# Optimization experiments

Measured on AMD Instinct MI355X. Metric: run time of the kernel, lower is better.

The kernel has to match this reference:

```python
import jax, jax.numpy as jnp
import numpy as np

N_NODES = 50000
D_IN = 256
D_OUT = 128
N_POS = 1600000   # positive edges used for GCN aggregation
N_PRED = 500000   # edges to score


def setup_inputs() -> dict:
    key = jax.random.key(0)
    ks = jax.random.split(key, 6)
    x = jax.random.normal(ks[0], (N_NODES, D_IN), dtype=jnp.float32)
    pos_edge_index = jax.random.randint(ks[1], (2, N_POS), 0, N_NODES)
    edge_index = jax.random.randint(ks[2], (2, N_PRED), 0, N_NODES)
    # init_linear: Linear(d_in, d_in); stored as (in, out) so fwd is x @ W1 + b1
    W1 = jax.random.normal(ks[3], (D_IN, D_IN), dtype=jnp.float32) / np.sqrt(D_IN).astype(np.float32)
    b1 = jnp.zeros((D_IN,), dtype=jnp.float32)
    # GCNConv weight (in, out) and bias
    Wc = jax.random.normal(ks[4], (D_IN, D_OUT), dtype=jnp.float32) / np.sqrt(D_IN).astype(np.float32)
    bc = jnp.zeros((D_OUT,), dtype=jnp.float32)
    return dict(x=x, edge_index=edge_index, pos_edge_index=pos_edge_index,
                W1=W1, b1=b1, Wc=Wc, bc=bc)


def reference(x, edge_index, pos_edge_index, W1, b1, Wc, bc):
    n = x.shape[0]
    # init_linear
    h = x @ W1 + b1                                  # [N, D_IN]
    # GCNConv: linear transform first, then normalized scatter-add aggregation
    h = h @ Wc                                       # [N, D_OUT]
    # add self-loops (PyG GCNConv default add_self_loops=True, edge_weight=1)
    loops = jnp.arange(n, dtype=pos_edge_index.dtype)
    row = jnp.concatenate([pos_edge_index[0], loops])  # source
    col = jnp.concatenate([pos_edge_index[1], loops])  # target (aggregation)
    # symmetric normalization: deg over target, norm = d^-1/2[row]*d^-1/2[col]
    deg = jax.ops.segment_sum(jnp.ones_like(col, dtype=h.dtype), col, num_segments=n)
    dinv = jnp.where(deg > 0, jax.lax.rsqrt(deg), 0.0)
    norm = dinv[row] * dinv[col]                     # [E+N]
    msgs = h[row] * norm[:, None]                    # gather + scale
    out = jax.ops.segment_sum(msgs, col, num_segments=n) + bc  # scatter-add + bias
    # edge dot-product scoring
    logits = (out[edge_index[0]] * out[edge_index[1]]).sum(axis=-1)  # [N_PRED]
    return logits
```

## Files before the change

kernel.cpp:

```cpp
#include <hip/hip_runtime.h>

#define N_NODES 50000
#define D_IN 256
#define D_OUT 128
#define N_POS 1600000
#define N_PRED 500000

#define G_BUCKETS 782
#define GPAD 1024
#define SB 640
#define CHUNK 2500
#define CAP 4096
#define GEMM_BLOCKS 782
#define QPRED 125000

#define NT 4
#define TSZ 12500
#define NPB 32
#define AGGB 1563

typedef __attribute__((ext_vector_type(8))) short short8;
typedef __attribute__((ext_vector_type(4))) float f32x4;

__device__ __forceinline__ unsigned short f2bf(float f) {
    unsigned int u = __float_as_uint(f);
    u += 0x7FFFu + ((u >> 16) & 1u);
    return (unsigned short)(u >> 16);
}
__device__ __forceinline__ unsigned int pk2(float a, float b) {
    unsigned int ua = __float_as_uint(a), ub = __float_as_uint(b);
    ua += 0x7FFFu + ((ua >> 16) & 1u);
    ub += 0x7FFFu + ((ub >> 16) & 1u);
    return (ua >> 16) | (ub & 0xFFFF0000u);
}
__device__ __forceinline__ float bflo(unsigned int u) { return __uint_as_float(u << 16); }
__device__ __forceinline__ float bfhi(unsigned int u) { return __uint_as_float(u & 0xFFFF0000u); }

__device__ __forceinline__ float dot8(uint4 ua, uint4 ub) {
    return bflo(ua.x) * bflo(ub.x) + bfhi(ua.x) * bfhi(ub.x)
         + bflo(ua.y) * bflo(ub.y) + bfhi(ua.y) * bfhi(ub.y)
         + bflo(ua.z) * bflo(ub.z) + bfhi(ua.z) * bfhi(ub.z)
         + bflo(ua.w) * bflo(ub.w) + bfhi(ua.w) * bfhi(ub.w);
}

__global__ void fuse_weights_k(const float* __restrict__ W1, const float* __restrict__ Wc,
                               const float* __restrict__ b1,
                               unsigned short* __restrict__ Bp, float* __restrict__ bf,
                               int* __restrict__ bfill) {
    if (blockIdx.x == 128) {
        for (int g = threadIdx.x; g < G_BUCKETS; g += 256) bfill[g] = g * CAP;
        return;
    }
    int gid = blockIdx.x * blockDim.x + threadIdx.x;
    int k = gid >> 7;
    int n = gid & 127;
    float acc = 0.f;
    #pragma unroll 4
    for (int kk = 0; kk < D_IN; ++kk)
        acc += W1[k * D_IN + kk] * Wc[kk * D_OUT + n];
    int ks = k >> 5, q = (k >> 3) & 3, jj = k & 7;
    int nt = n >> 4, nl = n & 15;
    int lane = q * 16 + nl;
    Bp[(((long)(ks * 8 + nt)) * 64 + lane) * 8 + jj] = f2bf(acc);
    if (gid < D_OUT) {
        float accb = 0.f;
        for (int kk = 0; kk < D_IN; ++kk)
            accb += b1[kk] * Wc[kk * D_OUT + gid];
        bf[gid] = accb;
    }
}

__global__ __launch_bounds__(256) void scatter_gemm_k(const int* __restrict__ row,
                                                      const int* __restrict__ col,
                                                      int* __restrict__ bfill,
                                                      unsigned int* __restrict__ eb,
                                                      const float* __restrict__ x,
                                                      const uint4* __restrict__ Bp,
                                                      const float* __restrict__ bf,
                                                      unsigned short* __restrict__ hsb) {
    __shared__ __align__(16) char smem[27456];
    if (blockIdx.x < GEMM_BLOCKS) {
        const int wave = threadIdx.x >> 6;
        const int lane = threadIdx.x & 63;
        const int q    = lane >> 4;
        const int ml   = lane & 15;
        const int m0   = blockIdx.x * 64 + wave * 16;

        f32x4 acc[8];
        #pragma unroll
        for (int t = 0; t < 8; ++t) acc[t] = (f32x4){0.f, 0.f, 0.f, 0.f};

        long arow = m0 + ml; if (arow > N_NODES - 1) arow = N_NODES - 1;
        const float* xrow = x + arow * D_IN + q * 8;

        #pragma unroll
        for (int ks = 0; ks < 8; ++ks) {
            float4 xa = *(const float4*)(xrow + ks * 32);
            float4 xb = *(const float4*)(xrow + ks * 32 + 4);
            union { short8 s; unsigned int u[4]; } af;
            af.u[0] = pk2(xa.x, xa.y);
            af.u[1] = pk2(xa.z, xa.w);
            af.u[2] = pk2(xb.x, xb.y);
            af.u[3] = pk2(xb.z, xb.w);
            #pragma unroll
            for (int nt = 0; nt < 8; ++nt) {
                union { uint4 v; short8 s; } bu;
                bu.v = Bp[(long)(ks * 8 + nt) * 64 + lane];
                acc[nt] = __builtin_amdgcn_mfma_f32_16x16x32_bf16(af.s, bu.s, acc[nt], 0, 0, 0);
            }
        }

        unsigned short* o = (unsigned short*)smem + wave * 2048;
        #pragma unroll
        for (int nt = 0; nt < 8; ++nt) {
            float bn = bf[nt * 16 + ml];
            #pragma unroll
            for (int r = 0; r < 4; ++r) {
                float val = acc[nt][r] + bn;
                o[(q * 4 + r) * 128 + nt * 16 + ml] = f2bf(val);
            }
        }
        __syncthreads();
        #pragma unroll
        for (int i = 0; i < 4; ++i) {
            int fb = i * 1024 + lane * 16;
            int v = m0 + (fb >> 8);
            if (v < N_NODES) {
                uint4 val = *(const uint4*)((const char*)o + fb);
                *(uint4*)((char*)hsb + (long)v * 256 + (fb & 255)) = val;
            }
        }
    } else {
        int* hist  = (int*)smem;
        int* lofs  = hist + GPAD;
        int* fill2 = lofs + GPAD;
        int* base  = fill2 + GPAD;
        int* part  = base + GPAD;
        unsigned int* stag = (unsigned int*)(part + 256);
        int t = threadIdx.x;
        for (int i = t; i < GPAD; i += 256) { hist[i] = 0; fill2[i] = 0; }
        __syncthreads();
        int e0 = (blockIdx.x - GEMM_BLOCKS) * CHUNK;
        for (int i = t; i < CHUNK; i += 256)
            atomicAdd(&hist[col[e0 + i] >> 6], 1);
        __syncthreads();
        int h[4], p4 = 0;
        #pragma unroll
        for (int i = 0; i < 4; ++i) { h[i] = hist[4 * t + i]; p4 += h[i]; }
        part[t] = p4;
        __syncthreads();
        for (int d = 1; d < 256; d <<= 1) {
            int add = (t >= d) ? part[t - d] : 0;
            __syncthreads();
            part[t] += add;
            __syncthreads();
        }
        int ex = part[t] - p4;
        #pragma unroll
        for (int i = 0; i < 4; ++i) { lofs[4 * t + i] = ex; ex += h[i]; }
        __syncthreads();
        for (int g = t; g < G_BUCKETS; g += 256) {
            int c = hist[g];
            base[g] = c ? atomicAdd(&bfill[g], c) : 0;
        }
        for (int i = t; i < CHUNK; i += 256) {
            int c = col[e0 + i];
            int g = c >> 6;
            unsigned int u = (unsigned int)row[e0 + i] | ((unsigned int)(c & 63) << 16)
                           | ((unsigned int)g << 22);
            int lp = atomicAdd(&fill2[g], 1);
            stag[lofs[g] + lp] = u;
        }
        __syncthreads();
        for (int i = t; i < CHUNK; i += 256) {
            unsigned int u = stag[i];
            int g = u >> 22;
            eb[base[g] + (i - lofs[g])] = u;
        }
    }
}

__global__ __launch_bounds__(256) void csr_build_k(const int* __restrict__ bfill,
                                                   const unsigned int* __restrict__ eb,
                                                   unsigned short* __restrict__ csr,
                                                   int* __restrict__ offs5,
                                                   float* __restrict__ dinv,
                                                   uint4* __restrict__ hsb4) {
    __shared__ unsigned int stag[CAP];
    __shared__ unsigned short stag2[CAP];
    __shared__ int hist[256], lofs[256], fill[256], part[256];
    __shared__ float dloc[64];
    int t = threadIdx.x;
    int g = blockIdx.x;
    int s = g * CAP;
    int cnt = bfill[g] - s;
    hist[t] = 0; fill[t] = 0;
    __syncthreads();
    for (int i = t; i < cnt; i += 256) {
        unsigned int u = eb[s + i];
        stag[i] = u;
        int r = u & 0xFFFF;
        int tile = (r >= TSZ) + (r >= 2 * TSZ) + (r >= 3 * TSZ);
        atomicAdd(&hist[((u >> 16) & 63) * NT + tile], 1);
    }
    __syncthreads();
    int hv = hist[t];
    part[t] = hv;
    __syncthreads();
    for (int d = 1; d < 256; d <<= 1) {
        int add = (t >= d) ? part[t - d] : 0;
        __syncthreads();
        part[t] += add;
        __syncthreads();
    }
    lofs[t] = part[t] - hv;
    __syncthreads();
    if (t < 64) {
        int v = g * 64 + t;
        int b4 = t * NT;
        int c0 = hist[b4], c1 = hist[b4 + 1], c2 = hist[b4 + 2], c3 = hist[b4 + 3];
        float dl = rsqrtf((float)(c0 + c1 + c2 + c3) + 1.0f);
        dloc[t] = dl;
        if (v < N_NODES) {
            int o0 = s + lofs[b4];
            offs5[v * 5 + 0] = o0;
            offs5[v * 5 + 1] = o0 + c0;
            offs5[v * 5 + 2] = o0 + c0 + c1;
            offs5[v * 5 + 3] = o0 + c0 + c1 + c2;
            offs5[v * 5 + 4] = o0 + c0 + c1 + c2 + c3;
            dinv[v] = dl;
        }
    }
    for (int i = t; i < cnt; i += 256) {
        unsigned int u = stag[i];
        int r = u & 0xFFFF;
        int tile = (r >= TSZ) + (r >= 2 * TSZ) + (r >= 3 * TSZ);
        int key = ((u >> 16) & 63) * NT + tile;
        int lp = atomicAdd(&fill[key], 1);
        stag2[lofs[key] + lp] = (unsigned short)r;
    }
    __syncthreads();
    for (int i = t; i < cnt; i += 256)
        csr[s + i] = stag2[i];
    const int vb = g * 64;
    for (int i = t; i < 64 * 16; i += 256) {
        int n = i >> 4;
        int v = vb + n;
        if (v < N_NODES) {
            float d = dloc[n];
            long idx = (long)v * 16 + (i & 15);
            uint4 u = hsb4[idx];
            uint4 o;
            o.x = pk2(d * bflo(u.x), d * bfhi(u.x));
            o.y = pk2(d * bflo(u.y), d * bfhi(u.y));
            o.z = pk2(d * bflo(u.z), d * bfhi(u.z));
            o.w = pk2(d * bflo(u.w), d * bfhi(u.w));
            hsb4[idx] = o;
        }
    }
}

__global__ __launch_bounds__(256, 8) void aggregate_csr_k(const int* __restrict__ offs5,
                                                          const unsigned short* __restrict__ csr,
                                                          const uint4* __restrict__ hs4,
                                                          const float* __restrict__ dinv,
                                                          const float* __restrict__ bc,
                                                          uint4* __restrict__ feat4) {
    int tid = threadIdx.x;
    int li  = tid & 15;
    int g16 = tid >> 4;
    int v0 = blockIdx.x * NPB + g16 * 2;
    int v1 = v0 + 1;
    bool ok0 = v0 < N_NODES, ok1 = v1 < N_NODES;

    float a0[8] = {0.f, 0.f, 0.f, 0.f, 0.f, 0.f, 0.f, 0.f};
    float a1[8] = {0.f, 0.f, 0.f, 0.f, 0.f, 0.f, 0.f, 0.f};

    #pragma unroll 1
    for (int tt = 0; tt < NT; ++tt) {
        if (ok0) {
            int i  = offs5[v0 * 5 + tt];
            int s1 = offs5[v0 * 5 + tt + 1];
            for (; i + 3 < s1; i += 4) {
                int r0 = csr[i], r1 = csr[i + 1], r2 = csr[i + 2], r3 = csr[i + 3];
                uint4 u0 = hs4[r0 * 16 + li];
                uint4 u1 = hs4[r1 * 16 + li];
                uint4 u2 = hs4[r2 * 16 + li];
                uint4 u3 = hs4[r3 * 16 + li];
                a0[0] += (bflo(u0.x) + bflo(u1.x)) + (bflo(u2.x) + bflo(u3.x));
                a0[1] += (bfhi(u0.x) + bfhi(u1.x)) + (bfhi(u2.x) + bfhi(u3.x));
                a0[2] += (bflo(u0.y) + bflo(u1.y)) + (bflo(u2.y) + bflo(u3.y));
                a0[3] += (bfhi(u0.y) + bfhi(u1.y)) + (bfhi(u2.y) + bfhi(u3.y));
                a0[4] += (bflo(u0.z) + bflo(u1.z)) + (bflo(u2.z) + bflo(u3.z));
                a0[5] += (bfhi(u0.z) + bfhi(u1.z)) + (bfhi(u2.z) + bfhi(u3.z));
                a0[6] += (bflo(u0.w) + bflo(u1.w)) + (bflo(u2.w) + bflo(u3.w));
                a0[7] += (bfhi(u0.w) + bfhi(u1.w)) + (bfhi(u2.w) + bfhi(u3.w));
            }
            for (; i < s1; ++i) {
                int r = csr[i];
                uint4 u = hs4[r * 16 + li];
                a0[0] += bflo(u.x); a0[1] += bfhi(u.x);
                a0[2] += bflo(u.y); a0[3] += bfhi(u.y);
                a0[4] += bflo(u.z); a0[5] += bfhi(u.z);
                a0[6] += bflo(u.w); a0[7] += bfhi(u.w);
            }
        }
        if (ok1) {
            int i  = offs5[v1 * 5 + tt];
            int s1 = offs5[v1 * 5 + tt + 1];
            for (; i + 3 < s1; i += 4) {
                int r0 = csr[i], r1 = csr[i + 1], r2 = csr[i + 2], r3 = csr[i + 3];
                uint4 u0 = hs4[r0 * 16 + li];
                uint4 u1 = hs4[r1 * 16 + li];
                uint4 u2 = hs4[r2 * 16 + li];
                uint4 u3 = hs4[r3 * 16 + li];
                a1[0] += (bflo(u0.x) + bflo(u1.x)) + (bflo(u2.x) + bflo(u3.x));
                a1[1] += (bfhi(u0.x) + bfhi(u1.x)) + (bfhi(u2.x) + bfhi(u3.x));
                a1[2] += (bflo(u0.y) + bflo(u1.y)) + (bflo(u2.y) + bflo(u3.y));
                a1[3] += (bfhi(u0.y) + bfhi(u1.y)) + (bfhi(u2.y) + bfhi(u3.y));
                a1[4] += (bflo(u0.z) + bflo(u1.z)) + (bflo(u2.z) + bflo(u3.z));
                a1[5] += (bfhi(u0.z) + bfhi(u1.z)) + (bfhi(u2.z) + bfhi(u3.z));
                a1[6] += (bflo(u0.w) + bflo(u1.w)) + (bflo(u2.w) + bflo(u3.w));
                a1[7] += (bfhi(u0.w) + bfhi(u1.w)) + (bfhi(u2.w) + bfhi(u3.w));
            }
            for (; i < s1; ++i) {
                int r = csr[i];
                uint4 u = hs4[r * 16 + li];
                a1[0] += bflo(u.x); a1[1] += bfhi(u.x);
                a1[2] += bflo(u.y); a1[3] += bfhi(u.y);
                a1[4] += bflo(u.z); a1[5] += bfhi(u.z);
                a1[6] += bflo(u.w); a1[7] += bfhi(u.w);
            }
        }
    }
    float4 b0 = *(const float4*)(bc + li * 8);
    float4 b1 = *(const float4*)(bc + li * 8 + 4);
    if (ok0) {
        uint4 su = hs4[(long)v0 * 16 + li];
        float dv = dinv[v0];
        float f0 = dv * (a0[0] + bflo(su.x)) + b0.x;
        float f1 = dv * (a0[1] + bfhi(su.x)) + b0.y;
        float f2 = dv * (a0[2] + bflo(su.y)) + b0.z;
        float f3 = dv * (a0[3] + bfhi(su.y)) + b0.w;
        float f4 = dv * (a0[4] + bflo(su.z)) + b1.x;
        float f5 = dv * (a0[5] + bfhi(su.z)) + b1.y;
        float f6 = dv * (a0[6] + bflo(su.w)) + b1.z;
        float f7 = dv * (a0[7] + bfhi(su.w)) + b1.w;
        uint4 o;
        o.x = pk2(f0, f1); o.y = pk2(f2, f3); o.z = pk2(f4, f5); o.w = pk2(f6, f7);
        feat4[(long)v0 * 16 + li] = o;
    }
    if (ok1) {
        uint4 su = hs4[(long)v1 * 16 + li];
        float dv = dinv[v1];
        float f0 = dv * (a1[0] + bflo(su.x)) + b0.x;
        float f1 = dv * (a1[1] + bfhi(su.x)) + b0.y;
        float f2 = dv * (a1[2] + bflo(su.y)) + b0.z;
        float f3 = dv * (a1[3] + bfhi(su.y)) + b0.w;
        float f4 = dv * (a1[4] + bflo(su.z)) + b1.x;
        float f5 = dv * (a1[5] + bfhi(su.z)) + b1.y;
        float f6 = dv * (a1[6] + bflo(su.w)) + b1.z;
        float f7 = dv * (a1[7] + bfhi(su.w)) + b1.w;
        uint4 o;
        o.x = pk2(f0, f1); o.y = pk2(f2, f3); o.z = pk2(f4, f5); o.w = pk2(f6, f7);
        feat4[(long)v1 * 16 + li] = o;
    }
}

__global__ void score_k(const int* __restrict__ src, const int* __restrict__ dst,
                        const uint4* __restrict__ feat4, float* __restrict__ out) {
    int gid = blockIdx.x * blockDim.x + threadIdx.x;
    int e = gid >> 4;
    int c = gid & 15;
    if (e >= QPRED) return;
    int e0 = e, e1 = e + QPRED, e2 = e + 2 * QPRED, e3 = e + 3 * QPRED;
    int a0 = src[e0], b0 = dst[e0];
    int a1 = src[e1], b1 = dst[e1];
    int a2 = src[e2], b2 = dst[e2];
    int a3 = src[e3], b3 = dst[e3];
    uint4 ua0 = feat4[(long)a0 * 16 + c];
    uint4 ub0 = feat4[(long)b0 * 16 + c];
    uint4 ua1 = feat4[(long)a1 * 16 + c];
    uint4 ub1 = feat4[(long)b1 * 16 + c];
    uint4 ua2 = feat4[(long)a2 * 16 + c];
    uint4 ub2 = feat4[(long)b2 * 16 + c];
    uint4 ua3 = feat4[(long)a3 * 16 + c];
    uint4 ub3 = feat4[(long)b3 * 16 + c];
    float p0 = dot8(ua0, ub0);
    float p1 = dot8(ua1, ub1);
    float p2 = dot8(ua2, ub2);
    float p3 = dot8(ua3, ub3);
    #pragma unroll
    for (int m = 8; m; m >>= 1) {
        p0 += __shfl_xor(p0, m, 16);
        p1 += __shfl_xor(p1, m, 16);
        p2 += __shfl_xor(p2, m, 16);
        p3 += __shfl_xor(p3, m, 16);
    }
    if (c == 0) {
        out[e0] = p0;
        out[e1] = p1;
        out[e2] = p2;
        out[e3] = p3;
    }
}

extern "C" void kernel_launch(void* const* d_in, const int* in_sizes, int n_in,
                              void* d_out, int out_size, void* d_ws, size_t ws_size,
                              hipStream_t stream) {
    const float* x   = (const float*)d_in[0];
    const int*   ei  = (const int*)  d_in[1];
    const int*   pe  = (const int*)  d_in[2];
    const float* W1  = (const float*)d_in[3];
    const float* b1  = (const float*)d_in[4];
    const float* Wc  = (const float*)d_in[5];
    const float* bc  = (const float*)d_in[6];
    float* out = (float*)d_out;

    const int* pe_row = pe;
    const int* pe_col = pe + N_POS;
    const int* ei_src = ei;
    const int* ei_dst = ei + N_PRED;

    char* w = (char*)d_ws;
    unsigned short* Bp = (unsigned short*)w;  w += 32768 * 2;
    float* bf    = (float*)w;                 w += 128 * 4;
    float* dinv  = (float*)w;                 w += 50000 * 4;
    int*   bfill = (int*)w;                   w += GPAD * 4;
    int*   offs5 = (int*)w;                   w += 50000 * 5 * 4;
    unsigned int* eb = (unsigned int*)w;      w += (long)G_BUCKETS * CAP * 4;
    unsigned short* csr = (unsigned short*)w; w += (long)G_BUCKETS * CAP * 2;
    unsigned short* hsb   = (unsigned short*)w;  w += (long)N_NODES * D_OUT * 2;
    unsigned short* featb = (unsigned short*)w;

    fuse_weights_k<<<129, 256, 0, stream>>>(W1, Wc, b1, Bp, bf, bfill);

    scatter_gemm_k<<<GEMM_BLOCKS + SB, 256, 0, stream>>>(pe_row, pe_col, bfill, eb,
                                                         x, (const uint4*)Bp, bf, hsb);

    csr_build_k   <<<G_BUCKETS, 256, 0, stream>>>(bfill, eb, csr, offs5, dinv,
                                                  (uint4*)hsb);

    aggregate_csr_k<<<AGGB, 256, 0, stream>>>(offs5, csr, (const uint4*)hsb,
                                              dinv, bc, (uint4*)featb);

    score_k       <<<(QPRED * 16 + 255) / 256, 256, 0, stream>>>(
                      ei_src, ei_dst, (const uint4*)featb, out);
}
```

Before: 238.2 us.

## Replace atomic bucket scatter with per-chunk segment table gathered in CSR build

The edge bucketing pass no longer reserves global space with atomicAdd on per-bucket fill counters and scatters edges into fixed-capacity buckets. Each scatter block now writes its locally sorted chunk contiguously, plus a per-(bucket, chunk) offset/count table. The CSR build kernel prefix-sums the counts and gathers each bucket's edges from all 640 chunks into shared memory. This removes the global atomics, the bfill init block, and the scattered global writes. The cost is that the CSR build does many small serial per-thread gather loops from different chunks, and the scatter blocks are now scheduled before the GEMM blocks.

Result: slower. 243.1 us (+2.1%).

```diff
diff --git a/kernel.cpp b/kernel.cpp
--- a/kernel.cpp
+++ b/kernel.cpp
@@ -45,12 +45,7 @@
 
 __global__ void fuse_weights_k(const float* __restrict__ W1, const float* __restrict__ Wc,
                                const float* __restrict__ b1,
-                               unsigned short* __restrict__ Bp, float* __restrict__ bf,
-                               int* __restrict__ bfill) {
-    if (blockIdx.x == 128) {
-        for (int g = threadIdx.x; g < G_BUCKETS; g += 256) bfill[g] = g * CAP;
-        return;
-    }
+                               unsigned short* __restrict__ Bp, float* __restrict__ bf) {
     int gid = blockIdx.x * blockDim.x + threadIdx.x;
     int k = gid >> 7;
     int n = gid & 127;
@@ -72,19 +67,61 @@
 
 __global__ __launch_bounds__(256) void scatter_gemm_k(const int* __restrict__ row,
                                                       const int* __restrict__ col,
-                                                      int* __restrict__ bfill,
-                                                      unsigned int* __restrict__ eb,
+                                                      unsigned int* __restrict__ seg,
+                                                      unsigned int* __restrict__ ebs,
                                                       const float* __restrict__ x,
                                                       const uint4* __restrict__ Bp,
                                                       const float* __restrict__ bf,
                                                       unsigned short* __restrict__ hsb) {
-    __shared__ __align__(16) char smem[27456];
-    if (blockIdx.x < GEMM_BLOCKS) {
+    __shared__ __align__(16) char smem[23424];
+    if (blockIdx.x < SB) {
+        int* hist  = (int*)smem;
+        int* lofs  = hist + GPAD;
+        int* fill2 = lofs + GPAD;
+        int* part  = fill2 + GPAD;
+        unsigned int* stag = (unsigned int*)(part + 256);
+        int t = threadIdx.x;
+        int b = blockIdx.x;
+        for (int i = t; i < GPAD; i += 256) { hist[i] = 0; fill2[i] = 0; }
+        __syncthreads();
+        int e0 = b * CHUNK;
+        for (int i = t; i < CHUNK; i += 256)
+            atomicAdd(&hist[col[e0 + i] >> 6], 1);
+        __syncthreads();
+        int h[4], p4 = 0;
+        #pragma unroll
+        for (int i = 0; i < 4; ++i) { h[i] = hist[4 * t + i]; p4 += h[i]; }
+        part[t] = p4;
+        __syncthreads();
+        for (int d = 1; d < 256; d <<= 1) {
+            int add = (t >= d) ? part[t - d] : 0;
+            __syncthreads();
+            part[t] += add;
+            __syncthreads();
+        }
+        int ex = part[t] - p4;
+        #pragma unroll
+        for (int i = 0; i < 4; ++i) { lofs[4 * t + i] = ex; ex += h[i]; }
+        __syncthreads();
+        for (int g = t; g < G_BUCKETS; g += 256)
+            seg[(long)g * SB + b] = (unsigned int)lofs[g] | ((unsigned int)hist[g] << 16);
+        for (int i = t; i < CHUNK; i += 256) {
+            int c = col[e0 + i];
+            int g = c >> 6;
+            unsigned int u = (unsigned int)row[e0 + i] | ((unsigned int)(c & 63) << 16);
+            int lp = atomicAdd(&fill2[g], 1);
+            stag[lofs[g] + lp] = u;
+        }
+        __syncthreads();
+        for (int i = t; i < CHUNK; i += 256)
+            ebs[(long)b * CHUNK + i] = stag[i];
+    } else {
+        const int gb   = blockIdx.x - SB;
         const int wave = threadIdx.x >> 6;
         const int lane = threadIdx.x & 63;
         const int q    = lane >> 4;
         const int ml   = lane & 15;
-        const int m0   = blockIdx.x * 64 + wave * 16;
+        const int m0   = gb * 64 + wave * 16;
 
         f32x4 acc[8];
         #pragma unroll
@@ -130,58 +167,11 @@
                 *(uint4*)((char*)hsb + (long)v * 256 + (fb & 255)) = val;
             }
         }
-    } else {
-        int* hist  = (int*)smem;
-        int* lofs  = hist + GPAD;
-        int* fill2 = lofs + GPAD;
-        int* base  = fill2 + GPAD;
-        int* part  = base + GPAD;
-        unsigned int* stag = (unsigned int*)(part + 256);
-        int t = threadIdx.x;
-        for (int i = t; i < GPAD; i += 256) { hist[i] = 0; fill2[i] = 0; }
-        __syncthreads();
-        int e0 = (blockIdx.x - GEMM_BLOCKS) * CHUNK;
-        for (int i = t; i < CHUNK; i += 256)
-            atomicAdd(&hist[col[e0 + i] >> 6], 1);
-        __syncthreads();
-        int h[4], p4 = 0;
-        #pragma unroll
-        for (int i = 0; i < 4; ++i) { h[i] = hist[4 * t + i]; p4 += h[i]; }
-        part[t] = p4;
-        __syncthreads();
-        for (int d = 1; d < 256; d <<= 1) {
-            int add = (t >= d) ? part[t - d] : 0;
-            __syncthreads();
-            part[t] += add;
-            __syncthreads();
-        }
-        int ex = part[t] - p4;
-        #pragma unroll
-        for (int i = 0; i < 4; ++i) { lofs[4 * t + i] = ex; ex += h[i]; }
-        __syncthreads();
-        for (int g = t; g < G_BUCKETS; g += 256) {
-            int c = hist[g];
-            base[g] = c ? atomicAdd(&bfill[g], c) : 0;
-        }
-        for (int i = t; i < CHUNK; i += 256) {
-            int c = col[e0 + i];
-            int g = c >> 6;
-            unsigned int u = (unsigned int)row[e0 + i] | ((unsigned int)(c & 63) << 16)
-                           | ((unsigned int)g << 22);
-            int lp = atomicAdd(&fill2[g], 1);
-            stag[lofs[g] + lp] = u;
-        }
-        __syncthreads();
-        for (int i = t; i < CHUNK; i += 256) {
-            unsigned int u = stag[i];
-            int g = u >> 22;
-            eb[base[g] + (i - lofs[g])] = u;
-        }
-    }
-}
-
-__global__ __launch_bounds__(256) void csr_build_k(const int* __restrict__ bfill,
-                                                   const unsigned int* __restrict__ eb,
+    }
+}
+
+__global__ __launch_bounds__(256) void csr_build_k(const unsigned int* __restrict__ seg,
+                                                   const unsigned int* __restrict__ ebs,
                                                    unsigned short* __restrict__ csr,
                                                    int* __restrict__ offs5,
                                                    float* __restrict__ dinv,
@@ -190,15 +180,41 @@
     __shared__ unsigned short stag2[CAP];
     __shared__ int hist[256], lofs[256], fill[256], part[256];
     __shared__ float dloc[64];
+    __shared__ int scnt;
     int t = threadIdx.x;
     int g = blockIdx.x;
     int s = g * CAP;
-    int cnt = bfill[g] - s;
     hist[t] = 0; fill[t] = 0;
-    __syncthreads();
+    const unsigned int* sg = seg + (long)g * SB;
+    unsigned int w0 = sg[t];
+    unsigned int w1 = sg[t + 256];
+    unsigned int w2 = (t + 512 < SB) ? sg[t + 512] : 0u;
+    int c0 = w0 >> 16, c1 = w1 >> 16, c2 = w2 >> 16;
+    int lsum = c0 + c1 + c2;
+    part[t] = lsum;
+    __syncthreads();
+    for (int d = 1; d < 256; d <<= 1) {
+        int add = (t >= d) ? part[t - d] : 0;
+        __syncthreads();
+        part[t] += add;
+        __syncthreads();
+    }
+    if (t == 255) scnt = part[255];
+    int p = part[t] - lsum;
+    {
+        const unsigned int* e0p = ebs + (long)t * CHUNK + (w0 & 0xFFFFu);
+        for (int k = 0; k < c0; ++k) stag[p + k] = e0p[k];
+        p += c0;
+        const unsigned int* e1p = ebs + (long)(t + 256) * CHUNK + (w1 & 0xFFFFu);
+        for (int k = 0; k < c1; ++k) stag[p + k] = e1p[k];
+        p += c1;
+        const unsigned int* e2p = ebs + (long)(t + 512) * CHUNK + (w2 & 0xFFFFu);
+        for (int k = 0; k < c2; ++k) stag[p + k] = e2p[k];
+    }
+    __syncthreads();
+    int cnt = scnt;
     for (int i = t; i < cnt; i += 256) {
-        unsigned int u = eb[s + i];
-        stag[i] = u;
+        unsigned int u = stag[i];
         int r = u & 0xFFFF;
         int tile = (r >= TSZ) + (r >= 2 * TSZ) + (r >= 3 * TSZ);
         atomicAdd(&hist[((u >> 16) & 63) * NT + tile], 1);
@@ -218,16 +234,16 @@
     if (t < 64) {
         int v = g * 64 + t;
         int b4 = t * NT;
-        int c0 = hist[b4], c1 = hist[b4 + 1], c2 = hist[b4 + 2], c3 = hist[b4 + 3];
-        float dl = rsqrtf((float)(c0 + c1 + c2 + c3) + 1.0f);
+        int cc0 = hist[b4], cc1 = hist[b4 + 1], cc2 = hist[b4 + 2], cc3 = hist[b4 + 3];
+        float dl = rsqrtf((float)(cc0 + cc1 + cc2 + cc3) + 1.0f);
         dloc[t] = dl;
         if (v < N_NODES) {
             int o0 = s + lofs[b4];
             offs5[v * 5 + 0] = o0;
-            offs5[v * 5 + 1] = o0 + c0;
-            offs5[v * 5 + 2] = o0 + c0 + c1;
-            offs5[v * 5 + 3] = o0 + c0 + c1 + c2;
-            offs5[v * 5 + 4] = o0 + c0 + c1 + c2 + c3;
+            offs5[v * 5 + 1] = o0 + cc0;
+            offs5[v * 5 + 2] = o0 + cc0 + cc1;
+            offs5[v * 5 + 3] = o0 + cc0 + cc1 + cc2;
+            offs5[v * 5 + 4] = o0 + cc0 + cc1 + cc2 + cc3;
             dinv[v] = dl;
         }
     }
@@ -426,19 +442,19 @@
     unsigned short* Bp = (unsigned short*)w;  w += 32768 * 2;
     float* bf    = (float*)w;                 w += 128 * 4;
     float* dinv  = (float*)w;                 w += 50000 * 4;
-    int*   bfill = (int*)w;                   w += GPAD * 4;
     int*   offs5 = (int*)w;                   w += 50000 * 5 * 4;
-    unsigned int* eb = (unsigned int*)w;      w += (long)G_BUCKETS * CAP * 4;
+    unsigned int* seg = (unsigned int*)w;     w += (long)G_BUCKETS * SB * 4;
+    unsigned int* ebs = (unsigned int*)w;     w += (long)SB * CHUNK * 4;
     unsigned short* csr = (unsigned short*)w; w += (long)G_BUCKETS * CAP * 2;
     unsigned short* hsb   = (unsigned short*)w;  w += (long)N_NODES * D_OUT * 2;
     unsigned short* featb = (unsigned short*)w;
 
-    fuse_weights_k<<<129, 256, 0, stream>>>(W1, Wc, b1, Bp, bf, bfill);
-
-    scatter_gemm_k<<<GEMM_BLOCKS + SB, 256, 0, stream>>>(pe_row, pe_col, bfill, eb,
+    fuse_weights_k<<<128, 256, 0, stream>>>(W1, Wc, b1, Bp, bf);
+
+    scatter_gemm_k<<<SB + GEMM_BLOCKS, 256, 0, stream>>>(pe_row, pe_col, seg, ebs,
                                                          x, (const uint4*)Bp, bf, hsb);
 
-    csr_build_k   <<<G_BUCKETS, 256, 0, stream>>>(bfill, eb, csr, offs5, dinv,
+    csr_build_k   <<<G_BUCKETS, 256, 0, stream>>>(seg, ebs, csr, offs5, dinv,
                                                   (uint4*)hsb);
 
     aggregate_csr_k<<<AGGB, 256, 0, stream>>>(offs5, csr, (const uint4*)hsb,
```
